# Kernel optimization log

Measured on AMD Instinct MI355X. Metric: run time of the kernel, lower is better.

## Reference

```python
import jax, jax.numpy as jnp
import numpy as np


def setup_inputs() -> dict:
    key0 = jax.random.key(0)
    kq, kk, kv = jax.random.split(key0, 3)
    B, S, D = 16, 2048, 64  # batch*heads, seq_len, head_dim
    return {
        "query": jax.random.normal(kq, (B, S, D), dtype=jnp.float32),
        "key": jax.random.normal(kk, (B, S, D), dtype=jnp.float32),
        "value": jax.random.normal(kv, (B, S, D), dtype=jnp.float32),
    }


def reference(query, key, value):
    # context = K @ V^T : [B, S, S]  (the seq x seq intermediate the kernel should avoid)
    context = jnp.einsum("bkd,bvd->bkv", key, value)
    # attention = context^T @ Q : [B, S, D]
    attention = jnp.einsum("bkv,bkd->bvd", context, query)
    return attention
```

## Files before the change

kernel.cpp:

```cpp
#include <hip/hip_runtime.h>


#define BATCH 16
#define SEQ   2048
#define DIM   64
#define SCHUNK 128
#define NCHUNK (SEQ / SCHUNK)
#define RBLK  64
#define VPAD  68

__global__ __launch_bounds__(256) void ktq_kernel(const float* __restrict__ K,
                                                  const float* __restrict__ Q,
                                                  float* __restrict__ M) {
    __shared__ float Ks[SCHUNK * DIM];
    __shared__ float Qs[SCHUNK * DIM];
    const int b     = blockIdx.y;
    const int chunk = blockIdx.x;
    const int t     = threadIdx.x;

    const float* Kb = K + (size_t)b * SEQ * DIM + (size_t)chunk * SCHUNK * DIM;
    const float* Qb = Q + (size_t)b * SEQ * DIM + (size_t)chunk * SCHUNK * DIM;

#pragma unroll
    for (int i = 0; i < 8; ++i) {
        int idx = i * 256 + t;
        ((float4*)Ks)[idx] = ((const float4*)Kb)[idx];
        ((float4*)Qs)[idx] = ((const float4*)Qb)[idx];
    }
    __syncthreads();

    const int tx = t & 15;
    const int ty = t >> 4;
    float acc[4][4];
#pragma unroll
    for (int i = 0; i < 4; ++i)
#pragma unroll
        for (int j = 0; j < 4; ++j) acc[i][j] = 0.f;

    for (int s = 0; s < SCHUNK; ++s) {
        float4 ak = *(const float4*)&Ks[s * DIM + ty * 4];
        float4 bq = *(const float4*)&Qs[s * DIM + tx * 4];
        float av[4] = {ak.x, ak.y, ak.z, ak.w};
        float bv[4] = {bq.x, bq.y, bq.z, bq.w};
#pragma unroll
        for (int i = 0; i < 4; ++i)
#pragma unroll
            for (int j = 0; j < 4; ++j) acc[i][j] += av[i] * bv[j];
    }

    float* Mb = M + b * DIM * DIM;
#pragma unroll
    for (int i = 0; i < 4; ++i)
#pragma unroll
        for (int j = 0; j < 4; ++j)
            atomicAdd(&Mb[(ty * 4 + i) * DIM + tx * 4 + j], acc[i][j]);
}

__global__ __launch_bounds__(256) void vm_kernel(const float* __restrict__ V,
                                                 const float* __restrict__ M,
                                                 float* __restrict__ O) {
    __shared__ float Ml[DIM * DIM];
    __shared__ float Vs[RBLK * VPAD];
    const int b  = blockIdx.y;
    const int rb = blockIdx.x;
    const int t  = threadIdx.x;

    const float* Mb = M + b * DIM * DIM;
    const float* Vb = V + (size_t)b * SEQ * DIM + (size_t)rb * RBLK * DIM;

#pragma unroll
    for (int i = 0; i < 4; ++i) {
        int idx = i * 256 + t;
        ((float4*)Ml)[idx] = ((const float4*)Mb)[idx];
    }
#pragma unroll
    for (int i = 0; i < 4; ++i) {
        int idx = i * 256 + t;
        int row = idx >> 4;
        int col = (idx & 15) * 4;
        float4 v = ((const float4*)Vb)[idx];
        *(float4*)&Vs[row * VPAD + col] = v;
    }
    __syncthreads();

    const int tx = t & 15;
    const int ty = t >> 4;
    float acc[4][4];
#pragma unroll
    for (int i = 0; i < 4; ++i)
#pragma unroll
        for (int j = 0; j < 4; ++j) acc[i][j] = 0.f;

    for (int dp = 0; dp < DIM; ++dp) {
        float4 mv = *(const float4*)&Ml[dp * DIM + tx * 4];
        float m[4] = {mv.x, mv.y, mv.z, mv.w};
        float a[4];
#pragma unroll
        for (int i = 0; i < 4; ++i) a[i] = Vs[(ty * 4 + i) * VPAD + dp];
#pragma unroll
        for (int i = 0; i < 4; ++i)
#pragma unroll
            for (int j = 0; j < 4; ++j) acc[i][j] += a[i] * m[j];
    }

    float* Ob = O + (size_t)b * SEQ * DIM + (size_t)rb * RBLK * DIM;
#pragma unroll
    for (int i = 0; i < 4; ++i) {
        float4 o = {acc[i][0], acc[i][1], acc[i][2], acc[i][3]};
        *(float4*)&Ob[(ty * 4 + i) * DIM + tx * 4] = o;
    }
}

extern "C" void kernel_launch(void* const* d_in, const int* in_sizes, int n_in,
                              void* d_out, int out_size, void* d_ws, size_t ws_size,
                              hipStream_t stream) {
    const float* Q = (const float*)d_in[0];
    const float* K = (const float*)d_in[1];
    const float* V = (const float*)d_in[2];
    float* O = (float*)d_out;
    float* M = (float*)d_ws;

    hipMemsetAsync(M, 0, (size_t)BATCH * DIM * DIM * sizeof(float), stream);

    dim3 gridA(NCHUNK, BATCH);
    ktq_kernel<<<gridA, 256, 0, stream>>>(K, Q, M);

    dim3 gridB(SEQ / RBLK, BATCH);
    vm_kernel<<<gridB, 256, 0, stream>>>(V, M, O);
}
```

Before: 99.50 us.

## Widen ktq blocks, transpose V in shared memory, use nontemporal loads/stores

ktq_kernel now runs 512 threads per block, each computing a 2x4 tile instead of 4x4, so more threads share the per-chunk work. vm_kernel stores V transposed in LDS so the inner loop reads one vector instead of four scalar strided reads. Global loads of K, Q and V and the output stores use nontemporal builtins to avoid cache pollution. The transposed scalar LDS writes may cause bank conflicts, and per-thread ILP in ktq drops.

```diff
diff --git a/kernel.cpp b/kernel.cpp
--- a/kernel.cpp
+++ b/kernel.cpp
@@ -1,5 +1,8 @@
 #include <hip/hip_runtime.h>
 
+
+typedef float vf4 __attribute__((ext_vector_type(4)));
+typedef float vf2 __attribute__((ext_vector_type(2)));
 
 #define BATCH 16
 #define SEQ   2048
@@ -7,9 +10,9 @@
 #define SCHUNK 128
 #define NCHUNK (SEQ / SCHUNK)
 #define RBLK  64
-#define VPAD  68
+#define TPAD  68
 
-__global__ __launch_bounds__(256) void ktq_kernel(const float* __restrict__ K,
+__global__ __launch_bounds__(512) void ktq_kernel(const float* __restrict__ K,
                                                   const float* __restrict__ Q,
                                                   float* __restrict__ M) {
     __shared__ float Ks[SCHUNK * DIM];
@@ -22,45 +25,43 @@
     const float* Qb = Q + (size_t)b * SEQ * DIM + (size_t)chunk * SCHUNK * DIM;
 
 #pragma unroll
-    for (int i = 0; i < 8; ++i) {
-        int idx = i * 256 + t;
-        ((float4*)Ks)[idx] = ((const float4*)Kb)[idx];
-        ((float4*)Qs)[idx] = ((const float4*)Qb)[idx];
+    for (int i = 0; i < 4; ++i) {
+        int idx = i * 512 + t;
+        ((vf4*)Ks)[idx] = __builtin_nontemporal_load(&((const vf4*)Kb)[idx]);
+        ((vf4*)Qs)[idx] = __builtin_nontemporal_load(&((const vf4*)Qb)[idx]);
     }
     __syncthreads();
 
     const int tx = t & 15;
     const int ty = t >> 4;
-    float acc[4][4];
+    float acc[2][4];
 #pragma unroll
-    for (int i = 0; i < 4; ++i)
+    for (int i = 0; i < 2; ++i)
 #pragma unroll
         for (int j = 0; j < 4; ++j) acc[i][j] = 0.f;
 
     for (int s = 0; s < SCHUNK; ++s) {
-        float4 ak = *(const float4*)&Ks[s * DIM + ty * 4];
-        float4 bq = *(const float4*)&Qs[s * DIM + tx * 4];
-        float av[4] = {ak.x, ak.y, ak.z, ak.w};
-        float bv[4] = {bq.x, bq.y, bq.z, bq.w};
+        vf2 ak = *(const vf2*)&Ks[s * DIM + ty * 2];
+        vf4 bq = *(const vf4*)&Qs[s * DIM + tx * 4];
 #pragma unroll
-        for (int i = 0; i < 4; ++i)
+        for (int i = 0; i < 2; ++i)
 #pragma unroll
-            for (int j = 0; j < 4; ++j) acc[i][j] += av[i] * bv[j];
+            for (int j = 0; j < 4; ++j) acc[i][j] += ak[i] * bq[j];
     }
 
     float* Mb = M + b * DIM * DIM;
 #pragma unroll
-    for (int i = 0; i < 4; ++i)
+    for (int i = 0; i < 2; ++i)
 #pragma unroll
         for (int j = 0; j < 4; ++j)
-            atomicAdd(&Mb[(ty * 4 + i) * DIM + tx * 4 + j], acc[i][j]);
+            atomicAdd(&Mb[(ty * 2 + i) * DIM + tx * 4 + j], acc[i][j]);
 }
 
 __global__ __launch_bounds__(256) void vm_kernel(const float* __restrict__ V,
                                                  const float* __restrict__ M,
                                                  float* __restrict__ O) {
     __shared__ float Ml[DIM * DIM];
-    __shared__ float Vs[RBLK * VPAD];
+    __shared__ float VsT[DIM * TPAD];
     const int b  = blockIdx.y;
     const int rb = blockIdx.x;
     const int t  = threadIdx.x;
@@ -71,15 +72,18 @@
 #pragma unroll
     for (int i = 0; i < 4; ++i) {
         int idx = i * 256 + t;
-        ((float4*)Ml)[idx] = ((const float4*)Mb)[idx];
+        ((vf4*)Ml)[idx] = ((const vf4*)Mb)[idx];
     }
 #pragma unroll
     for (int i = 0; i < 4; ++i) {
         int idx = i * 256 + t;
         int row = idx >> 4;
         int col = (idx & 15) * 4;
-        float4 v = ((const float4*)Vb)[idx];
-        *(float4*)&Vs[row * VPAD + col] = v;
+        vf4 v = __builtin_nontemporal_load(&((const vf4*)Vb)[idx]);
+        VsT[(col + 0) * TPAD + row] = v[0];
+        VsT[(col + 1) * TPAD + row] = v[1];
+        VsT[(col + 2) * TPAD + row] = v[2];
+        VsT[(col + 3) * TPAD + row] = v[3];
     }
     __syncthreads();
 
@@ -92,22 +96,19 @@
         for (int j = 0; j < 4; ++j) acc[i][j] = 0.f;
 
     for (int dp = 0; dp < DIM; ++dp) {
-        float4 mv = *(const float4*)&Ml[dp * DIM + tx * 4];
-        float m[4] = {mv.x, mv.y, mv.z, mv.w};
-        float a[4];
-#pragma unroll
-        for (int i = 0; i < 4; ++i) a[i] = Vs[(ty * 4 + i) * VPAD + dp];
+        vf4 mv = *(const vf4*)&Ml[dp * DIM + tx * 4];
+        vf4 av = *(const vf4*)&VsT[dp * TPAD + ty * 4];
 #pragma unroll
         for (int i = 0; i < 4; ++i)
 #pragma unroll
-            for (int j = 0; j < 4; ++j) acc[i][j] += a[i] * m[j];
+            for (int j = 0; j < 4; ++j) acc[i][j] += av[i] * mv[j];
     }
 
     float* Ob = O + (size_t)b * SEQ * DIM + (size_t)rb * RBLK * DIM;
 #pragma unroll
     for (int i = 0; i < 4; ++i) {
-        float4 o = {acc[i][0], acc[i][1], acc[i][2], acc[i][3]};
-        *(float4*)&Ob[(ty * 4 + i) * DIM + tx * 4] = o;
+        vf4 o = {acc[i][0], acc[i][1], acc[i][2], acc[i][3]};
+        __builtin_nontemporal_store(o, (vf4*)&Ob[(ty * 4 + i) * DIM + tx * 4]);
     }
 }
 
@@ -120,10 +121,10 @@
     float* O = (float*)d_out;
     float* M = (float*)d_ws;
 
-    hipMemsetAsync(M, 0, (size_t)BATCH * DIM * DIM * sizeof(float), stream);
+    (void)hipMemsetAsync(M, 0, (size_t)BATCH * DIM * DIM * sizeof(float), stream);
 
     dim3 gridA(NCHUNK, BATCH);
-    ktq_kernel<<<gridA, 256, 0, stream>>>(K, Q, M);
+    ktq_kernel<<<gridA, 512, 0, stream>>>(K, Q, M);
 
     dim3 gridB(SEQ / RBLK, BATCH);
     vm_kernel<<<gridB, 256, 0, stream>>>(V, M, O);
```

Result: slower. 104.5 us (+5.0%).
